# Performance work log

Measured on AMD Instinct MI355X. Metric: run time of the kernel, lower is better.

The kernel has to match this reference:

```python
import jax, jax.numpy as jnp
import numpy as np
from math import pi

N = 262144
OUT_RES = 512
OUT_CHANNELS = 64
EPS = 3.33  # out_res in [177, 890)
SQ2PI = 2.50662827463


def make_sphere_pos(out_res, eps):
    # Fibonacci sphere lattice, matches the torch buffer construction.
    indices = jnp.arange(out_res, dtype=jnp.float32)
    golden_ratio = (1 + 5 ** 0.5) / 2
    phi = jnp.arccos(1 - 2 * (indices + eps) / (out_res - 1 + 2 * eps))
    theta = 2 * pi * indices / golden_ratio
    x = jnp.cos(theta) * jnp.sin(phi)
    y = jnp.sin(theta) * jnp.sin(phi)
    z = jnp.cos(phi)
    return jnp.stack([x, y, z], axis=0).astype(jnp.float32)  # [3, out_res]


def setup_inputs() -> dict:
    key = jax.random.key(0)
    k1, k2 = jax.random.split(key)
    vec = jax.random.normal(k1, (N, 3), dtype=jnp.float32)
    vec = vec / (jnp.linalg.norm(vec, axis=-1, keepdims=True) + 1e-8)  # unit directions
    weights = jax.random.uniform(k2, (1, OUT_RES, OUT_CHANNELS), dtype=jnp.float32)
    sphere_pos = make_sphere_pos(OUT_RES, EPS)
    sigma = jnp.full((1,), 0.1, dtype=jnp.float32)
    return {"vec": vec, "sphere_pos": sphere_pos, "weights": weights, "sigma": sigma}


def reference(vec, sphere_pos, weights, sigma):
    # cos_dist: [N, out_res]
    cos_dist = jnp.clip(vec @ sphere_pos, -1 + 1e-5, 1 - 1e-5)
    ang = jnp.arccos(cos_dist)
    prob = jnp.exp(-(ang / sigma) ** 2 / 2) / SQ2PI / sigma  # gaussian of geodesic dist
    prob = prob / (prob.sum(axis=1, keepdims=True) + 1e-8)
    # [N, out_res] @ [out_res, out_channels] -> [N, out_channels]
    return prob @ weights[0]
```

## Files before the change

kernel.cpp:

```cpp
#include <hip/hip_runtime.h>
#include <math.h>

typedef short bf16x8 __attribute__((ext_vector_type(8)));
typedef float f32x4  __attribute__((ext_vector_type(4)));

__device__ __forceinline__ unsigned short f2bf_rne(float x) {
  union { float f; unsigned u; } a; a.f = x;
  unsigned r = a.u + 0x7fffu + ((a.u >> 16) & 1u);
  return (unsigned short)(r >> 16);
}

__device__ __forceinline__ float fast_exp2(float x) {
#if __has_builtin(__builtin_amdgcn_exp2f)
  return __builtin_amdgcn_exp2f(x);
#else
  float r; asm("v_exp_f32 %0, %1" : "=v"(r) : "v"(x)); return r;
#endif
}

__device__ __forceinline__ unsigned cvt_pk_bf16(float a, float b) {
  unsigned r; asm("v_cvt_pk_bf16_f32 %0, %1, %2" : "=v"(r) : "v"(a), "v"(b)); return r;
}

__device__ __forceinline__ int zkey(float vz) {
  int k = (int)((1.0f - vz) * 128.0f);
  return min(max(k, 0), 255);
}

__global__ void hist_k(const float* __restrict__ vec, int* __restrict__ cnt, int rpb) {
  __shared__ int h[256];
  h[threadIdx.x] = 0;
  __syncthreads();
  const int base = blockIdx.x * rpb;
  for (int t = threadIdx.x; t < rpb; t += 256)
    atomicAdd(&h[zkey(vec[(base + t) * 3 + 2])], 1);
  __syncthreads();
  cnt[blockIdx.x * 256 + threadIdx.x] = h[threadIdx.x];
}

__global__ void scanA_k(const int* __restrict__ cnt, int* __restrict__ basem,
                        int* __restrict__ tot) {
  __shared__ int s[256];
  const int bin = blockIdx.x, t = threadIdx.x;
  const int v = cnt[t * 256 + bin];
  s[t] = v;
  __syncthreads();
  int acc = v;
  #pragma unroll
  for (int off = 1; off < 256; off <<= 1) {
    const int other = (t >= off) ? s[t - off] : 0;
    __syncthreads();
    acc += other;
    s[t] = acc;
    __syncthreads();
  }
  basem[t * 256 + bin] = acc - v;
  if (t == 255) tot[bin] = acc;
}

__global__ void scatter_k(const float* __restrict__ vec, const int* __restrict__ basem,
                          const int* __restrict__ tot, int* __restrict__ perm,
                          int rpb) {
  __shared__ int s[256];
  __shared__ int bb[256];
  __shared__ int l[256];
  const int t = threadIdx.x;
  const int v = tot[t];
  s[t] = v;
  l[t] = 0;
  __syncthreads();
  int acc = v;
  #pragma unroll
  for (int off = 1; off < 256; off <<= 1) {
    const int other = (t >= off) ? s[t - off] : 0;
    __syncthreads();
    acc += other;
    s[t] = acc;
    __syncthreads();
  }
  bb[t] = acc - v;
  __syncthreads();
  const int base = blockIdx.x * rpb;
  for (int i0 = t; i0 < rpb; i0 += 256) {
    const int i = base + i0;
    const int k = zkey(vec[i * 3 + 2]);
    const int r = atomicAdd(&l[k], 1);
    perm[bb[k] + basem[blockIdx.x * 256 + k] + r] = i;
  }
}

__global__ __launch_bounds__(1024, 4) void sph_enc_sorted(
    const float* __restrict__ vec,
    const float* __restrict__ sph,
    const float* __restrict__ wts,
    const float* __restrict__ sigp,
    const int*   __restrict__ perm,
    float* __restrict__ out)
{
  __shared__ __align__(16) unsigned char wlds[64 * 512 * 2];
  __shared__ __align__(16) float slds[3 * 512];

  const int tid  = threadIdx.x;
  const int lane = tid & 63;
  const int wave = tid >> 6;

  for (int i = tid; i < 1536; i += 1024) slds[i] = sph[i];

  {
    const int c    = tid & 63;
    const int kgrp = tid >> 6;
    const int swz  = (c & 7) << 4;
    #pragma unroll
    for (int pass = 0; pass < 4; ++pass) {
      const int k0 = pass * 128 + (kgrp << 3);
      unsigned pk[4];
      #pragma unroll
      for (int i = 0; i < 4; ++i) {
        const unsigned lo = f2bf_rne(wts[(k0 + 2 * i)     * 64 + c]);
        const unsigned hi = f2bf_rne(wts[(k0 + 2 * i + 1) * 64 + c]);
        pk[i] = lo | (hi << 16);
      }
      *reinterpret_cast<uint4*>(wlds + (((c << 10) + (k0 << 1)) ^ swz)) =
          make_uint4(pk[0], pk[1], pk[2], pk[3]);
    }
  }
  __syncthreads();

  const float sigma = sigp[0];
  const float C1 = -1.44269504f / (sigma * sigma);
  const float C2 = C1 * 0.16666667f;
  const float K2 = -__log2f(2.50662827463f * sigma);

  const int r16  = lane & 15;
  const int q    = lane >> 4;

  const int g     = (blockIdx.x << 4) + wave;
  const int seg   = ((g & 15) << 9) + (g >> 4);
  const int sbase = seg << 5;
  const int p0 = perm[sbase + r16];
  const int p1 = perm[sbase + 16 + r16];

  const float vx0 = vec[p0 * 3 + 0], vy0 = vec[p0 * 3 + 1], vz0 = vec[p0 * 3 + 2];
  const float vx1 = vec[p1 * 3 + 0], vy1 = vec[p1 * 3 + 1], vz1 = vec[p1 * 3 + 2];
  const float nvx0 = -vx0, nvy0 = -vy0, nvz0 = -vz0;
  const float nvx1 = -vx1, nvy1 = -vy1, nvz1 = -vz1;

  const float thm = fminf(4.0f * sigma, 3.14159f);
  const float ct = __cosf(thm), st = __sinf(thm);
  const float s0 = sqrtf(fmaxf(0.0f, 1.0f - vz0 * vz0));
  const float s1 = sqrtf(fmaxf(0.0f, 1.0f - vz1 * vz1));
  float zh = fmaxf(fmaf(vz0, ct, s0 * st), fmaf(vz1, ct, s1 * st));
  float zl = fminf(fmaf(vz0, ct, -s0 * st), fmaf(vz1, ct, -s1 * st));
  #pragma unroll
  for (int m = 1; m < 64; m <<= 1) {
    zh = fmaxf(zh, __shfl_xor(zh, m));
    zl = fminf(zl, __shfl_xor(zl, m));
  }
  const float Dl = 511.0f + 2.0f * 3.33f;
  const float fi_lo = (1.0f - zh) * (0.5f * Dl) - 3.33f - 1.5f;
  const float fi_hi = (1.0f - zl) * (0.5f * Dl) - 3.33f + 1.5f;
  const int ilo = (int)fmaxf(fi_lo, 0.0f);
  const int ihi = (int)fminf(fi_hi, 511.0f);
  const int kt_lo = ilo >> 5;
  const int kt_hi = (ihi >> 5) + 1;

  f32x4 acc0[4], acc1[4];
  #pragma unroll
  for (int nb = 0; nb < 4; ++nb) {
    acc0[nb] = (f32x4){0.f, 0.f, 0.f, 0.f};
    acc1[nb] = (f32x4){0.f, 0.f, 0.f, 0.f};
  }
  float rsa0 = 0.f, rsb0 = 0.f, rsa1 = 0.f, rsb1 = 0.f;

  const int swz_r = (lane & 7) << 4;

  for (int kt = kt_lo; kt < kt_hi; ++kt) {
    const int j0 = kt * 32 + q * 8;
    union { bf16x8 v; unsigned u32[4]; } af0, af1;

    #pragma unroll
    for (int h = 0; h < 2; ++h) {
      const int jh = j0 + 4 * h;
      const f32x4 X = *reinterpret_cast<const f32x4*>(&slds[jh]);
      const f32x4 Y = *reinterpret_cast<const f32x4*>(&slds[512 + jh]);
      const f32x4 Z = *reinterpret_cast<const f32x4*>(&slds[1024 + jh]);
      float p[4];
      #pragma unroll
      for (int e = 0; e < 4; ++e) {
        const float u = fmaf(nvx0, X[e], fmaf(nvy0, Y[e], fmaf(nvz0, Z[e], 1.0f)));
        p[e] = fast_exp2(fmaf(u, fmaf(u, C2, C1), K2));
      }
      rsa0 += p[0] + p[2];
      rsb0 += p[1] + p[3];
      af0.u32[2 * h]     = cvt_pk_bf16(p[0], p[1]);
      af0.u32[2 * h + 1] = cvt_pk_bf16(p[2], p[3]);
      #pragma unroll
      for (int e = 0; e < 4; ++e) {
        const float u = fmaf(nvx1, X[e], fmaf(nvy1, Y[e], fmaf(nvz1, Z[e], 1.0f)));
        p[e] = fast_exp2(fmaf(u, fmaf(u, C2, C1), K2));
      }
      rsa1 += p[0] + p[2];
      rsb1 += p[1] + p[3];
      af1.u32[2 * h]     = cvt_pk_bf16(p[0], p[1]);
      af1.u32[2 * h + 1] = cvt_pk_bf16(p[2], p[3]);
    }

    const int kbyte = j0 << 1;
    #pragma unroll
    for (int nb = 0; nb < 4; ++nb) {
      const bf16x8 bf = *reinterpret_cast<const bf16x8*>(
          wlds + (((((nb << 4) + r16) << 10) + kbyte) ^ swz_r));
      acc0[nb] = __builtin_amdgcn_mfma_f32_16x16x32_bf16(af0.v, bf, acc0[nb], 0, 0, 0);
      acc1[nb] = __builtin_amdgcn_mfma_f32_16x16x32_bf16(af1.v, bf, acc1[nb], 0, 0, 0);
    }
  }

  float rsum0 = rsa0 + rsb0;
  float rsum1 = rsa1 + rsb1;
  rsum0 += __shfl_xor(rsum0, 16);
  rsum0 += __shfl_xor(rsum0, 32);
  rsum1 += __shfl_xor(rsum1, 16);
  rsum1 += __shfl_xor(rsum1, 32);

  #pragma unroll
  for (int reg = 0; reg < 4; ++reg) {
    const int orow = (q << 2) + reg;
    const float rinv0 = 1.0f / (__shfl(rsum0, orow) + 1e-8f);
    const float rinv1 = 1.0f / (__shfl(rsum1, orow) + 1e-8f);
    const int r0 = perm[sbase + orow];
    const int r1 = perm[sbase + 16 + orow];
    const int b0 = (r0 << 6) + r16;
    const int b1 = (r1 << 6) + r16;
    out[b0 +  0] = acc0[0][reg] * rinv0;
    out[b0 + 16] = acc0[1][reg] * rinv0;
    out[b0 + 32] = acc0[2][reg] * rinv0;
    out[b0 + 48] = acc0[3][reg] * rinv0;
    out[b1 +  0] = acc1[0][reg] * rinv1;
    out[b1 + 16] = acc1[1][reg] * rinv1;
    out[b1 + 32] = acc1[2][reg] * rinv1;
    out[b1 + 48] = acc1[3][reg] * rinv1;
  }
}

__global__ __launch_bounds__(1024, 4) void sph_enc_kernel(
    const float* __restrict__ vec,
    const float* __restrict__ sph,
    const float* __restrict__ wts,
    const float* __restrict__ sigp,
    float* __restrict__ out)
{
  __shared__ __align__(16) unsigned char wlds[64 * 512 * 2];
  __shared__ __align__(16) float slds[3 * 512];

  const int tid  = threadIdx.x;
  const int lane = tid & 63;
  const int wave = tid >> 6;

  for (int i = tid; i < 1536; i += 1024) slds[i] = sph[i];
  {
    const int c    = tid & 63;
    const int kgrp = tid >> 6;
    const int swz  = (c & 7) << 4;
    #pragma unroll
    for (int pass = 0; pass < 4; ++pass) {
      const int k0 = pass * 128 + (kgrp << 3);
      unsigned pk[4];
      #pragma unroll
      for (int i = 0; i < 4; ++i) {
        const unsigned lo = f2bf_rne(wts[(k0 + 2 * i)     * 64 + c]);
        const unsigned hi = f2bf_rne(wts[(k0 + 2 * i + 1) * 64 + c]);
        pk[i] = lo | (hi << 16);
      }
      *reinterpret_cast<uint4*>(wlds + (((c << 10) + (k0 << 1)) ^ swz)) =
          make_uint4(pk[0], pk[1], pk[2], pk[3]);
    }
  }
  __syncthreads();

  const float sigma = sigp[0];
  const float C1 = -1.44269504f / (sigma * sigma);
  const float C2 = C1 * 0.16666667f;
  const float K2 = -__log2f(2.50662827463f * sigma);

  const int r16  = lane & 15;
  const int q    = lane >> 4;
  const int row0 = (blockIdx.x << 9) + (wave << 4) + r16;
  const int row1 = row0 + 256;

  const float nvx0 = -vec[row0 * 3 + 0];
  const float nvy0 = -vec[row0 * 3 + 1];
  const float nvz0 = -vec[row0 * 3 + 2];
  const float nvx1 = -vec[row1 * 3 + 0];
  const float nvy1 = -vec[row1 * 3 + 1];
  const float nvz1 = -vec[row1 * 3 + 2];

  f32x4 acc0[4], acc1[4];
  #pragma unroll
  for (int nb = 0; nb < 4; ++nb) {
    acc0[nb] = (f32x4){0.f, 0.f, 0.f, 0.f};
    acc1[nb] = (f32x4){0.f, 0.f, 0.f, 0.f};
  }
  float rsa0 = 0.f, rsb0 = 0.f, rsa1 = 0.f, rsb1 = 0.f;
  const int swz_r = (lane & 7) << 4;

  #pragma unroll
  for (int kt = 0; kt < 16; ++kt) {
    const int j0 = kt * 32 + q * 8;
    union { bf16x8 v; unsigned u32[4]; } af0, af1;
    #pragma unroll
    for (int h = 0; h < 2; ++h) {
      const int jh = j0 + 4 * h;
      const f32x4 X = *reinterpret_cast<const f32x4*>(&slds[jh]);
      const f32x4 Y = *reinterpret_cast<const f32x4*>(&slds[512 + jh]);
      const f32x4 Z = *reinterpret_cast<const f32x4*>(&slds[1024 + jh]);
      float p[4];
      #pragma unroll
      for (int e = 0; e < 4; ++e) {
        const float u = fmaf(nvx0, X[e], fmaf(nvy0, Y[e], fmaf(nvz0, Z[e], 1.0f)));
        p[e] = fast_exp2(fmaf(u, fmaf(u, C2, C1), K2));
      }
      rsa0 += p[0] + p[2];
      rsb0 += p[1] + p[3];
      af0.u32[2 * h]     = cvt_pk_bf16(p[0], p[1]);
      af0.u32[2 * h + 1] = cvt_pk_bf16(p[2], p[3]);
      #pragma unroll
      for (int e = 0; e < 4; ++e) {
        const float u = fmaf(nvx1, X[e], fmaf(nvy1, Y[e], fmaf(nvz1, Z[e], 1.0f)));
        p[e] = fast_exp2(fmaf(u, fmaf(u, C2, C1), K2));
      }
      rsa1 += p[0] + p[2];
      rsb1 += p[1] + p[3];
      af1.u32[2 * h]     = cvt_pk_bf16(p[0], p[1]);
      af1.u32[2 * h + 1] = cvt_pk_bf16(p[2], p[3]);
    }
    const int kbyte = j0 << 1;
    #pragma unroll
    for (int nb = 0; nb < 4; ++nb) {
      const bf16x8 bf = *reinterpret_cast<const bf16x8*>(
          wlds + (((((nb << 4) + r16) << 10) + kbyte) ^ swz_r));
      acc0[nb] = __builtin_amdgcn_mfma_f32_16x16x32_bf16(af0.v, bf, acc0[nb], 0, 0, 0);
      acc1[nb] = __builtin_amdgcn_mfma_f32_16x16x32_bf16(af1.v, bf, acc1[nb], 0, 0, 0);
    }
  }

  float rsum0 = rsa0 + rsb0;
  float rsum1 = rsa1 + rsb1;
  rsum0 += __shfl_xor(rsum0, 16);
  rsum0 += __shfl_xor(rsum0, 32);
  rsum1 += __shfl_xor(rsum1, 16);
  rsum1 += __shfl_xor(rsum1, 32);

  const int obase = (blockIdx.x << 9) + (wave << 4);
  #pragma unroll
  for (int reg = 0; reg < 4; ++reg) {
    const int orow = (q << 2) + reg;
    const float rinv0 = 1.0f / (__shfl(rsum0, orow) + 1e-8f);
    const float rinv1 = 1.0f / (__shfl(rsum1, orow) + 1e-8f);
    const int b0 = ((obase + orow) << 6) + r16;
    const int b1 = ((obase + 256 + orow) << 6) + r16;
    out[b0 +  0] = acc0[0][reg] * rinv0;
    out[b0 + 16] = acc0[1][reg] * rinv0;
    out[b0 + 32] = acc0[2][reg] * rinv0;
    out[b0 + 48] = acc0[3][reg] * rinv0;
    out[b1 +  0] = acc1[0][reg] * rinv1;
    out[b1 + 16] = acc1[1][reg] * rinv1;
    out[b1 + 32] = acc1[2][reg] * rinv1;
    out[b1 + 48] = acc1[3][reg] * rinv1;
  }
}

extern "C" void kernel_launch(void* const* d_in, const int* in_sizes, int n_in,
                              void* d_out, int out_size, void* d_ws, size_t ws_size,
                              hipStream_t stream) {
  const float* vec = (const float*)d_in[0];
  const float* sph = (const float*)d_in[1];
  const float* wts = (const float*)d_in[2];
  const float* sig = (const float*)d_in[3];
  float* out = (float*)d_out;
  const int n = in_sizes[0] / 3;

  const size_t need = ((size_t)n + 65536 + 65536 + 256) * sizeof(int);
  if (n == 262144 && ws_size >= need) {
    int* perm    = (int*)d_ws;
    int* cnt     = perm + n;
    int* basem   = cnt + 65536;
    int* tot     = basem + 65536;
    const int rpb = n / 256;
    hipLaunchKernelGGL(hist_k,    dim3(256), dim3(256), 0, stream, vec, cnt, rpb);
    hipLaunchKernelGGL(scanA_k,   dim3(256), dim3(256), 0, stream, cnt, basem, tot);
    hipLaunchKernelGGL(scatter_k, dim3(256), dim3(256), 0, stream, vec, basem, tot, perm, rpb);
    hipLaunchKernelGGL(sph_enc_sorted, dim3(n >> 9), dim3(1024), 0, stream,
                       vec, sph, wts, sig, perm, out);
  } else {
    hipLaunchKernelGGL(sph_enc_kernel, dim3(n >> 9), dim3(1024), 0, stream,
                       vec, sph, wts, sig, out);
  }
}
```

Measured before the change: 46.62 us.

## Merge scan into scatter and precompute swizzled bf16 weights once

Removes the separate scanA kernel: each scatter block now sums the 256 per-block histogram counts itself to get its bin offsets and totals. This cuts one launch at the cost of redundant column reads of cnt in every block. The bf16 conversion and swizzle of the weights moves into the histogram kernel and is written once to workspace. The 512 main-kernel blocks then copy pre-packed uint4s into LDS instead of each redoing the strided fp32 loads and conversion.

```diff
diff --git a/kernel.cpp b/kernel.cpp
--- a/kernel.cpp
+++ b/kernel.cpp
@@ -27,72 +27,77 @@
   return min(max(k, 0), 255);
 }
 
-__global__ void hist_k(const float* __restrict__ vec, int* __restrict__ cnt, int rpb) {
+__global__ void hist_prep_k(const float* __restrict__ vec, int* __restrict__ cnt,
+                            const float* __restrict__ wts, unsigned char* __restrict__ wbf,
+                            int rpb) {
   __shared__ int h[256];
   h[threadIdx.x] = 0;
   __syncthreads();
   const int base = blockIdx.x * rpb;
   for (int t = threadIdx.x; t < rpb; t += 256)
     atomicAdd(&h[zkey(vec[(base + t) * 3 + 2])], 1);
+
+  const int gt = blockIdx.x * 256 + threadIdx.x;
+  if (gt < 4096) {
+    const int c  = gt >> 6;
+    const int k0 = (gt & 63) << 3;
+    unsigned pk[4];
+    #pragma unroll
+    for (int i = 0; i < 4; ++i) {
+      const unsigned lo = f2bf_rne(wts[(k0 + 2 * i)     * 64 + c]);
+      const unsigned hi = f2bf_rne(wts[(k0 + 2 * i + 1) * 64 + c]);
+      pk[i] = lo | (hi << 16);
+    }
+    const int swz = (c & 7) << 4;
+    *reinterpret_cast<uint4*>(wbf + (((c << 10) + (k0 << 1)) ^ swz)) =
+        make_uint4(pk[0], pk[1], pk[2], pk[3]);
+  }
   __syncthreads();
   cnt[blockIdx.x * 256 + threadIdx.x] = h[threadIdx.x];
 }
 
-__global__ void scanA_k(const int* __restrict__ cnt, int* __restrict__ basem,
-                        int* __restrict__ tot) {
+__global__ void scatter2_k(const float* __restrict__ vec, const int* __restrict__ cnt,
+                           int* __restrict__ perm, int rpb) {
   __shared__ int s[256];
-  const int bin = blockIdx.x, t = threadIdx.x;
-  const int v = cnt[t * 256 + bin];
-  s[t] = v;
-  __syncthreads();
-  int acc = v;
+  __shared__ int bb[256];
+  __shared__ int bm[256];
+  __shared__ int l[256];
+  const int t   = threadIdx.x;
+  const int blk = blockIdx.x;
+  int partial = 0, total = 0;
+  for (int b = 0; b < 256; ++b) {
+    const int v = cnt[b * 256 + t];
+    partial += (b < blk) ? v : 0;
+    total   += v;
+  }
+  s[t] = total;
+  bm[t] = partial;
+  l[t] = 0;
+  __syncthreads();
+  int acc = total;
   #pragma unroll
   for (int off = 1; off < 256; off <<= 1) {
-    const int other = (t >= off) ? s[t - off] : 0;
+    const int o = (t >= off) ? s[t - off] : 0;
     __syncthreads();
-    acc += other;
+    acc += o;
     s[t] = acc;
     __syncthreads();
   }
-  basem[t * 256 + bin] = acc - v;
-  if (t == 255) tot[bin] = acc;
-}
-
-__global__ void scatter_k(const float* __restrict__ vec, const int* __restrict__ basem,
-                          const int* __restrict__ tot, int* __restrict__ perm,
-                          int rpb) {
-  __shared__ int s[256];
-  __shared__ int bb[256];
-  __shared__ int l[256];
-  const int t = threadIdx.x;
-  const int v = tot[t];
-  s[t] = v;
-  l[t] = 0;
-  __syncthreads();
-  int acc = v;
-  #pragma unroll
-  for (int off = 1; off < 256; off <<= 1) {
-    const int other = (t >= off) ? s[t - off] : 0;
-    __syncthreads();
-    acc += other;
-    s[t] = acc;
-    __syncthreads();
-  }
-  bb[t] = acc - v;
-  __syncthreads();
-  const int base = blockIdx.x * rpb;
+  bb[t] = acc - total;
+  __syncthreads();
+  const int base = blk * rpb;
   for (int i0 = t; i0 < rpb; i0 += 256) {
     const int i = base + i0;
     const int k = zkey(vec[i * 3 + 2]);
     const int r = atomicAdd(&l[k], 1);
-    perm[bb[k] + basem[blockIdx.x * 256 + k] + r] = i;
+    perm[bb[k] + bm[k] + r] = i;
   }
 }
 
 __global__ __launch_bounds__(1024, 4) void sph_enc_sorted(
     const float* __restrict__ vec,
     const float* __restrict__ sph,
-    const float* __restrict__ wts,
+    const unsigned char* __restrict__ wbf,
     const float* __restrict__ sigp,
     const int*   __restrict__ perm,
     float* __restrict__ out)
@@ -107,22 +112,10 @@
   for (int i = tid; i < 1536; i += 1024) slds[i] = sph[i];
 
   {
-    const int c    = tid & 63;
-    const int kgrp = tid >> 6;
-    const int swz  = (c & 7) << 4;
-    #pragma unroll
-    for (int pass = 0; pass < 4; ++pass) {
-      const int k0 = pass * 128 + (kgrp << 3);
-      unsigned pk[4];
-      #pragma unroll
-      for (int i = 0; i < 4; ++i) {
-        const unsigned lo = f2bf_rne(wts[(k0 + 2 * i)     * 64 + c]);
-        const unsigned hi = f2bf_rne(wts[(k0 + 2 * i + 1) * 64 + c]);
-        pk[i] = lo | (hi << 16);
-      }
-      *reinterpret_cast<uint4*>(wlds + (((c << 10) + (k0 << 1)) ^ swz)) =
-          make_uint4(pk[0], pk[1], pk[2], pk[3]);
-    }
+    const uint4* wsrc = reinterpret_cast<const uint4*>(wbf);
+    uint4* wdst = reinterpret_cast<uint4*>(wlds);
+    #pragma unroll
+    for (int i = 0; i < 4; ++i) wdst[i * 1024 + tid] = wsrc[i * 1024 + tid];
   }
   __syncthreads();
 
@@ -379,18 +372,16 @@
   float* out = (float*)d_out;
   const int n = in_sizes[0] / 3;
 
-  const size_t need = ((size_t)n + 65536 + 65536 + 256) * sizeof(int);
+  const size_t need = ((size_t)n + 65536) * sizeof(int) + 65536;
   if (n == 262144 && ws_size >= need) {
-    int* perm    = (int*)d_ws;
-    int* cnt     = perm + n;
-    int* basem   = cnt + 65536;
-    int* tot     = basem + 65536;
+    int* perm = (int*)d_ws;
+    int* cnt  = perm + n;
+    unsigned char* wbf = (unsigned char*)(cnt + 65536);
     const int rpb = n / 256;
-    hipLaunchKernelGGL(hist_k,    dim3(256), dim3(256), 0, stream, vec, cnt, rpb);
-    hipLaunchKernelGGL(scanA_k,   dim3(256), dim3(256), 0, stream, cnt, basem, tot);
-    hipLaunchKernelGGL(scatter_k, dim3(256), dim3(256), 0, stream, vec, basem, tot, perm, rpb);
+    hipLaunchKernelGGL(hist_prep_k, dim3(256), dim3(256), 0, stream, vec, cnt, wts, wbf, rpb);
+    hipLaunchKernelGGL(scatter2_k,  dim3(256), dim3(256), 0, stream, vec, cnt, perm, rpb);
     hipLaunchKernelGGL(sph_enc_sorted, dim3(n >> 9), dim3(1024), 0, stream,
-                       vec, sph, wts, sig, perm, out);
+                       vec, sph, wbf, sig, perm, out);
   } else {
     hipLaunchKernelGGL(sph_enc_kernel, dim3(n >> 9), dim3(1024), 0, stream,
                        vec, sph, wts, sig, out);
```

Result: slower. 53.12 us (+13.9%).

## Fuse sort passes and encoder into one cooperative kernel with grid syncs

Applied to the files above, without the earlier changes.

Merges the histogram, scan, scatter and sorted encoder kernels into a single cooperative launch of 256 blocks of 1024 threads. Grid-wide barriers separate the phases, and each block then handles two wave-groups of the encoder work in a loop. The aim is to remove three extra kernel launches and their gaps. In exchange it adds grid.sync costs, halves the encoder grid to 256 blocks, and risks occupancy or cooperative-launch limits given the 64 KB LDS per block.

```diff
diff --git a/kernel.cpp b/kernel.cpp
--- a/kernel.cpp
+++ b/kernel.cpp
@@ -1,5 +1,8 @@
 #include <hip/hip_runtime.h>
+#include <hip/hip_cooperative_groups.h>
 #include <math.h>
+
+namespace cg = cooperative_groups;
 
 typedef short bf16x8 __attribute__((ext_vector_type(8)));
 typedef float f32x4  __attribute__((ext_vector_type(4)));
@@ -27,85 +30,81 @@
   return min(max(k, 0), 255);
 }
 
-__global__ void hist_k(const float* __restrict__ vec, int* __restrict__ cnt, int rpb) {
-  __shared__ int h[256];
-  h[threadIdx.x] = 0;
-  __syncthreads();
-  const int base = blockIdx.x * rpb;
-  for (int t = threadIdx.x; t < rpb; t += 256)
-    atomicAdd(&h[zkey(vec[(base + t) * 3 + 2])], 1);
-  __syncthreads();
-  cnt[blockIdx.x * 256 + threadIdx.x] = h[threadIdx.x];
-}
-
-__global__ void scanA_k(const int* __restrict__ cnt, int* __restrict__ basem,
-                        int* __restrict__ tot) {
-  __shared__ int s[256];
-  const int bin = blockIdx.x, t = threadIdx.x;
-  const int v = cnt[t * 256 + bin];
-  s[t] = v;
-  __syncthreads();
-  int acc = v;
-  #pragma unroll
-  for (int off = 1; off < 256; off <<= 1) {
-    const int other = (t >= off) ? s[t - off] : 0;
-    __syncthreads();
-    acc += other;
-    s[t] = acc;
-    __syncthreads();
-  }
-  basem[t * 256 + bin] = acc - v;
-  if (t == 255) tot[bin] = acc;
-}
-
-__global__ void scatter_k(const float* __restrict__ vec, const int* __restrict__ basem,
-                          const int* __restrict__ tot, int* __restrict__ perm,
-                          int rpb) {
-  __shared__ int s[256];
-  __shared__ int bb[256];
-  __shared__ int l[256];
-  const int t = threadIdx.x;
-  const int v = tot[t];
-  s[t] = v;
-  l[t] = 0;
-  __syncthreads();
-  int acc = v;
-  #pragma unroll
-  for (int off = 1; off < 256; off <<= 1) {
-    const int other = (t >= off) ? s[t - off] : 0;
-    __syncthreads();
-    acc += other;
-    s[t] = acc;
-    __syncthreads();
-  }
-  bb[t] = acc - v;
-  __syncthreads();
-  const int base = blockIdx.x * rpb;
-  for (int i0 = t; i0 < rpb; i0 += 256) {
-    const int i = base + i0;
-    const int k = zkey(vec[i * 3 + 2]);
-    const int r = atomicAdd(&l[k], 1);
-    perm[bb[k] + basem[blockIdx.x * 256 + k] + r] = i;
-  }
-}
-
-__global__ __launch_bounds__(1024, 4) void sph_enc_sorted(
+__global__ __launch_bounds__(1024, 4) void fused_k(
     const float* __restrict__ vec,
     const float* __restrict__ sph,
     const float* __restrict__ wts,
     const float* __restrict__ sigp,
-    const int*   __restrict__ perm,
+    int* __restrict__ perm,
+    int* __restrict__ cnt,
+    int* __restrict__ basem,
+    int* __restrict__ tot,
     float* __restrict__ out)
 {
+  cg::grid_group grid = cg::this_grid();
+
   __shared__ __align__(16) unsigned char wlds[64 * 512 * 2];
   __shared__ __align__(16) float slds[3 * 512];
+  __shared__ int s[256];
+  __shared__ int h[256];
+  __shared__ int bb[256];
 
   const int tid  = threadIdx.x;
+  const int blk  = blockIdx.x;
   const int lane = tid & 63;
   const int wave = tid >> 6;
 
+  if (tid < 256) h[tid] = 0;
+  __syncthreads();
+  {
+    const int i = (blk << 10) + tid;
+    atomicAdd(&h[zkey(vec[i * 3 + 2])], 1);
+  }
+  __syncthreads();
+  if (tid < 256) cnt[(blk << 8) + tid] = h[tid];
+  grid.sync();
+
+  {
+    int v = 0;
+    if (tid < 256) { v = cnt[(tid << 8) + blk]; s[tid] = v; }
+    __syncthreads();
+    int acc = v;
+    for (int off = 1; off < 256; off <<= 1) {
+      int o = 0;
+      if (tid < 256 && tid >= off) o = s[tid - off];
+      __syncthreads();
+      if (tid < 256) { acc += o; s[tid] = acc; }
+      __syncthreads();
+    }
+    if (tid < 256) {
+      basem[(tid << 8) + blk] = acc - v;
+      if (tid == 255) tot[blk] = acc;
+    }
+  }
+  grid.sync();
+
+  {
+    int v = 0;
+    if (tid < 256) { v = tot[tid]; s[tid] = v; h[tid] = 0; }
+    __syncthreads();
+    int acc = v;
+    for (int off = 1; off < 256; off <<= 1) {
+      int o = 0;
+      if (tid < 256 && tid >= off) o = s[tid - off];
+      __syncthreads();
+      if (tid < 256) { acc += o; s[tid] = acc; }
+      __syncthreads();
+    }
+    if (tid < 256) bb[tid] = acc - v;
+    __syncthreads();
+    const int i = (blk << 10) + tid;
+    const int k = zkey(vec[i * 3 + 2]);
+    const int r = atomicAdd(&h[k], 1);
+    perm[bb[k] + basem[(blk << 8) + k] + r] = i;
+  }
+  grid.sync();
+
   for (int i = tid; i < 1536; i += 1024) slds[i] = sph[i];
-
   {
     const int c    = tid & 63;
     const int kgrp = tid >> 6;
@@ -131,114 +130,115 @@
   const float C2 = C1 * 0.16666667f;
   const float K2 = -__log2f(2.50662827463f * sigma);
 
-  const int r16  = lane & 15;
-  const int q    = lane >> 4;
-
-  const int g     = (blockIdx.x << 4) + wave;
-  const int seg   = ((g & 15) << 9) + (g >> 4);
-  const int sbase = seg << 5;
-  const int p0 = perm[sbase + r16];
-  const int p1 = perm[sbase + 16 + r16];
-
-  const float vx0 = vec[p0 * 3 + 0], vy0 = vec[p0 * 3 + 1], vz0 = vec[p0 * 3 + 2];
-  const float vx1 = vec[p1 * 3 + 0], vy1 = vec[p1 * 3 + 1], vz1 = vec[p1 * 3 + 2];
-  const float nvx0 = -vx0, nvy0 = -vy0, nvz0 = -vz0;
-  const float nvx1 = -vx1, nvy1 = -vy1, nvz1 = -vz1;
-
-  const float thm = fminf(4.0f * sigma, 3.14159f);
-  const float ct = __cosf(thm), st = __sinf(thm);
-  const float s0 = sqrtf(fmaxf(0.0f, 1.0f - vz0 * vz0));
-  const float s1 = sqrtf(fmaxf(0.0f, 1.0f - vz1 * vz1));
-  float zh = fmaxf(fmaf(vz0, ct, s0 * st), fmaf(vz1, ct, s1 * st));
-  float zl = fminf(fmaf(vz0, ct, -s0 * st), fmaf(vz1, ct, -s1 * st));
-  #pragma unroll
-  for (int m = 1; m < 64; m <<= 1) {
-    zh = fmaxf(zh, __shfl_xor(zh, m));
-    zl = fminf(zl, __shfl_xor(zl, m));
-  }
-  const float Dl = 511.0f + 2.0f * 3.33f;
-  const float fi_lo = (1.0f - zh) * (0.5f * Dl) - 3.33f - 1.5f;
-  const float fi_hi = (1.0f - zl) * (0.5f * Dl) - 3.33f + 1.5f;
-  const int ilo = (int)fmaxf(fi_lo, 0.0f);
-  const int ihi = (int)fminf(fi_hi, 511.0f);
-  const int kt_lo = ilo >> 5;
-  const int kt_hi = (ihi >> 5) + 1;
-
-  f32x4 acc0[4], acc1[4];
-  #pragma unroll
-  for (int nb = 0; nb < 4; ++nb) {
-    acc0[nb] = (f32x4){0.f, 0.f, 0.f, 0.f};
-    acc1[nb] = (f32x4){0.f, 0.f, 0.f, 0.f};
-  }
-  float rsa0 = 0.f, rsb0 = 0.f, rsa1 = 0.f, rsb1 = 0.f;
-
+  const int r16   = lane & 15;
+  const int q     = lane >> 4;
   const int swz_r = (lane & 7) << 4;
 
-  for (int kt = kt_lo; kt < kt_hi; ++kt) {
-    const int j0 = kt * 32 + q * 8;
-    union { bf16x8 v; unsigned u32[4]; } af0, af1;
-
-    #pragma unroll
-    for (int h = 0; h < 2; ++h) {
-      const int jh = j0 + 4 * h;
-      const f32x4 X = *reinterpret_cast<const f32x4*>(&slds[jh]);
-      const f32x4 Y = *reinterpret_cast<const f32x4*>(&slds[512 + jh]);
-      const f32x4 Z = *reinterpret_cast<const f32x4*>(&slds[1024 + jh]);
-      float p[4];
-      #pragma unroll
-      for (int e = 0; e < 4; ++e) {
-        const float u = fmaf(nvx0, X[e], fmaf(nvy0, Y[e], fmaf(nvz0, Z[e], 1.0f)));
-        p[e] = fast_exp2(fmaf(u, fmaf(u, C2, C1), K2));
-      }
-      rsa0 += p[0] + p[2];
-      rsb0 += p[1] + p[3];
-      af0.u32[2 * h]     = cvt_pk_bf16(p[0], p[1]);
-      af0.u32[2 * h + 1] = cvt_pk_bf16(p[2], p[3]);
-      #pragma unroll
-      for (int e = 0; e < 4; ++e) {
-        const float u = fmaf(nvx1, X[e], fmaf(nvy1, Y[e], fmaf(nvz1, Z[e], 1.0f)));
-        p[e] = fast_exp2(fmaf(u, fmaf(u, C2, C1), K2));
-      }
-      rsa1 += p[0] + p[2];
-      rsb1 += p[1] + p[3];
-      af1.u32[2 * h]     = cvt_pk_bf16(p[0], p[1]);
-      af1.u32[2 * h + 1] = cvt_pk_bf16(p[2], p[3]);
-    }
-
-    const int kbyte = j0 << 1;
+  for (int it = 0; it < 2; ++it) {
+    const int g     = (it << 12) + (blk << 4) + wave;
+    const int seg   = ((g & 15) << 9) + (g >> 4);
+    const int sbase = seg << 5;
+    const int p0 = perm[sbase + r16];
+    const int p1 = perm[sbase + 16 + r16];
+
+    const float vx0 = vec[p0 * 3 + 0], vy0 = vec[p0 * 3 + 1], vz0 = vec[p0 * 3 + 2];
+    const float vx1 = vec[p1 * 3 + 0], vy1 = vec[p1 * 3 + 1], vz1 = vec[p1 * 3 + 2];
+    const float nvx0 = -vx0, nvy0 = -vy0, nvz0 = -vz0;
+    const float nvx1 = -vx1, nvy1 = -vy1, nvz1 = -vz1;
+
+    const float thm = fminf(4.0f * sigma, 3.14159f);
+    const float ct = __cosf(thm), st = __sinf(thm);
+    const float s0 = sqrtf(fmaxf(0.0f, 1.0f - vz0 * vz0));
+    const float s1 = sqrtf(fmaxf(0.0f, 1.0f - vz1 * vz1));
+    float zh = fmaxf(fmaf(vz0, ct, s0 * st), fmaf(vz1, ct, s1 * st));
+    float zl = fminf(fmaf(vz0, ct, -s0 * st), fmaf(vz1, ct, -s1 * st));
+    #pragma unroll
+    for (int m = 1; m < 64; m <<= 1) {
+      zh = fmaxf(zh, __shfl_xor(zh, m));
+      zl = fminf(zl, __shfl_xor(zl, m));
+    }
+    const float Dl = 511.0f + 2.0f * 3.33f;
+    const float fi_lo = (1.0f - zh) * (0.5f * Dl) - 3.33f - 1.5f;
+    const float fi_hi = (1.0f - zl) * (0.5f * Dl) - 3.33f + 1.5f;
+    const int ilo = (int)fmaxf(fi_lo, 0.0f);
+    const int ihi = (int)fminf(fi_hi, 511.0f);
+    const int kt_lo = ilo >> 5;
+    const int kt_hi = (ihi >> 5) + 1;
+
+    f32x4 acc0[4], acc1[4];
     #pragma unroll
     for (int nb = 0; nb < 4; ++nb) {
-      const bf16x8 bf = *reinterpret_cast<const bf16x8*>(
-          wlds + (((((nb << 4) + r16) << 10) + kbyte) ^ swz_r));
-      acc0[nb] = __builtin_amdgcn_mfma_f32_16x16x32_bf16(af0.v, bf, acc0[nb], 0, 0, 0);
-      acc1[nb] = __builtin_amdgcn_mfma_f32_16x16x32_bf16(af1.v, bf, acc1[nb], 0, 0, 0);
-    }
-  }
-
-  float rsum0 = rsa0 + rsb0;
-  float rsum1 = rsa1 + rsb1;
-  rsum0 += __shfl_xor(rsum0, 16);
-  rsum0 += __shfl_xor(rsum0, 32);
-  rsum1 += __shfl_xor(rsum1, 16);
-  rsum1 += __shfl_xor(rsum1, 32);
-
-  #pragma unroll
-  for (int reg = 0; reg < 4; ++reg) {
-    const int orow = (q << 2) + reg;
-    const float rinv0 = 1.0f / (__shfl(rsum0, orow) + 1e-8f);
-    const float rinv1 = 1.0f / (__shfl(rsum1, orow) + 1e-8f);
-    const int r0 = perm[sbase + orow];
-    const int r1 = perm[sbase + 16 + orow];
-    const int b0 = (r0 << 6) + r16;
-    const int b1 = (r1 << 6) + r16;
-    out[b0 +  0] = acc0[0][reg] * rinv0;
-    out[b0 + 16] = acc0[1][reg] * rinv0;
-    out[b0 + 32] = acc0[2][reg] * rinv0;
-    out[b0 + 48] = acc0[3][reg] * rinv0;
-    out[b1 +  0] = acc1[0][reg] * rinv1;
-    out[b1 + 16] = acc1[1][reg] * rinv1;
-    out[b1 + 32] = acc1[2][reg] * rinv1;
-    out[b1 + 48] = acc1[3][reg] * rinv1;
+      acc0[nb] = (f32x4){0.f, 0.f, 0.f, 0.f};
+      acc1[nb] = (f32x4){0.f, 0.f, 0.f, 0.f};
+    }
+    float rsa0 = 0.f, rsb0 = 0.f, rsa1 = 0.f, rsb1 = 0.f;
+
+    for (int kt = kt_lo; kt < kt_hi; ++kt) {
+      const int j0 = kt * 32 + q * 8;
+      union { bf16x8 v; unsigned u32[4]; } af0, af1;
+
+      #pragma unroll
+      for (int hh = 0; hh < 2; ++hh) {
+        const int jh = j0 + 4 * hh;
+        const f32x4 X = *reinterpret_cast<const f32x4*>(&slds[jh]);
+        const f32x4 Y = *reinterpret_cast<const f32x4*>(&slds[512 + jh]);
+        const f32x4 Z = *reinterpret_cast<const f32x4*>(&slds[1024 + jh]);
+        float p[4];
+        #pragma unroll
+        for (int e = 0; e < 4; ++e) {
+          const float u = fmaf(nvx0, X[e], fmaf(nvy0, Y[e], fmaf(nvz0, Z[e], 1.0f)));
+          p[e] = fast_exp2(fmaf(u, fmaf(u, C2, C1), K2));
+        }
+        rsa0 += p[0] + p[2];
+        rsb0 += p[1] + p[3];
+        af0.u32[2 * hh]     = cvt_pk_bf16(p[0], p[1]);
+        af0.u32[2 * hh + 1] = cvt_pk_bf16(p[2], p[3]);
+        #pragma unroll
+        for (int e = 0; e < 4; ++e) {
+          const float u = fmaf(nvx1, X[e], fmaf(nvy1, Y[e], fmaf(nvz1, Z[e], 1.0f)));
+          p[e] = fast_exp2(fmaf(u, fmaf(u, C2, C1), K2));
+        }
+        rsa1 += p[0] + p[2];
+        rsb1 += p[1] + p[3];
+        af1.u32[2 * hh]     = cvt_pk_bf16(p[0], p[1]);
+        af1.u32[2 * hh + 1] = cvt_pk_bf16(p[2], p[3]);
+      }
+
+      const int kbyte = j0 << 1;
+      #pragma unroll
+      for (int nb = 0; nb < 4; ++nb) {
+        const bf16x8 bf = *reinterpret_cast<const bf16x8*>(
+            wlds + (((((nb << 4) + r16) << 10) + kbyte) ^ swz_r));
+        acc0[nb] = __builtin_amdgcn_mfma_f32_16x16x32_bf16(af0.v, bf, acc0[nb], 0, 0, 0);
+        acc1[nb] = __builtin_amdgcn_mfma_f32_16x16x32_bf16(af1.v, bf, acc1[nb], 0, 0, 0);
+      }
+    }
+
+    float rsum0 = rsa0 + rsb0;
+    float rsum1 = rsa1 + rsb1;
+    rsum0 += __shfl_xor(rsum0, 16);
+    rsum0 += __shfl_xor(rsum0, 32);
+    rsum1 += __shfl_xor(rsum1, 16);
+    rsum1 += __shfl_xor(rsum1, 32);
+
+    #pragma unroll
+    for (int reg = 0; reg < 4; ++reg) {
+      const int orow = (q << 2) + reg;
+      const float rinv0 = 1.0f / (__shfl(rsum0, orow) + 1e-8f);
+      const float rinv1 = 1.0f / (__shfl(rsum1, orow) + 1e-8f);
+      const int r0 = perm[sbase + orow];
+      const int r1 = perm[sbase + 16 + orow];
+      const int b0 = (r0 << 6) + r16;
+      const int b1 = (r1 << 6) + r16;
+      out[b0 +  0] = acc0[0][reg] * rinv0;
+      out[b0 + 16] = acc0[1][reg] * rinv0;
+      out[b0 + 32] = acc0[2][reg] * rinv0;
+      out[b0 + 48] = acc0[3][reg] * rinv0;
+      out[b1 +  0] = acc1[0][reg] * rinv1;
+      out[b1 + 16] = acc1[1][reg] * rinv1;
+      out[b1 + 32] = acc1[2][reg] * rinv1;
+      out[b1 + 48] = acc1[3][reg] * rinv1;
+    }
   }
 }
 
@@ -381,16 +381,14 @@
 
   const size_t need = ((size_t)n + 65536 + 65536 + 256) * sizeof(int);
   if (n == 262144 && ws_size >= need) {
-    int* perm    = (int*)d_ws;
-    int* cnt     = perm + n;
-    int* basem   = cnt + 65536;
-    int* tot     = basem + 65536;
-    const int rpb = n / 256;
-    hipLaunchKernelGGL(hist_k,    dim3(256), dim3(256), 0, stream, vec, cnt, rpb);
-    hipLaunchKernelGGL(scanA_k,   dim3(256), dim3(256), 0, stream, cnt, basem, tot);
-    hipLaunchKernelGGL(scatter_k, dim3(256), dim3(256), 0, stream, vec, basem, tot, perm, rpb);
-    hipLaunchKernelGGL(sph_enc_sorted, dim3(n >> 9), dim3(1024), 0, stream,
-                       vec, sph, wts, sig, perm, out);
+    int* perm  = (int*)d_ws;
+    int* cnt   = perm + n;
+    int* basem = cnt + 65536;
+    int* tot   = basem + 65536;
+    void* args[] = {(void*)&vec, (void*)&sph, (void*)&wts, (void*)&sig,
+                    (void*)&perm, (void*)&cnt, (void*)&basem, (void*)&tot, (void*)&out};
+    hipLaunchCooperativeKernel(reinterpret_cast<void*>(fused_k),
+                               dim3(256), dim3(1024), args, 0, stream);
   } else {
     hipLaunchKernelGGL(sph_enc_kernel, dim3(n >> 9), dim3(1024), 0, stream,
                        vec, sph, wts, sig, out);
```

Measured after the change: 133.2 us. 2.86x slower.
